# Kernel optimization log

Measured on AMD Instinct MI355X. Metric: run time of the kernel, lower is better.

Reference implementation:

```python
import jax, jax.numpy as jnp
from jax import lax
import numpy as np

NUM_HEAD = 4
D_MODEL = 160
HEAD_DIM = D_MODEL // NUM_HEAD  # 40
FEAT_DIM = 64
F_SIZE = (128, 128)
B = 4
LN_EPS = 1e-5
LEAKY_SLOPE = 0.01
DN = ('NCHW', 'OIHW', 'NCHW')


def setup_inputs() -> dict:
    key = jax.random.key(0)
    ks = jax.random.split(key, 10)
    pe_len = (F_SIZE[0] // 2) * (F_SIZE[1] // 2) + 1  # 4097
    s = 0.05
    return {
        'x': jax.random.normal(ks[0], (B, FEAT_DIM, F_SIZE[0], F_SIZE[1]), jnp.float32),
        'conv1_w': jax.random.normal(ks[1], (FEAT_DIM, FEAT_DIM, 2, 2), jnp.float32) * s,
        'conv1_b': jax.random.normal(ks[2], (FEAT_DIM,), jnp.float32) * s,
        'conv2_w': jax.random.normal(ks[3], (D_MODEL, FEAT_DIM, 1, 1), jnp.float32) * s,
        'conv2_b': jax.random.normal(ks[4], (D_MODEL,), jnp.float32) * s,
        'pe': jax.random.uniform(ks[5], (pe_len, 1), jnp.float32),
        'wq': jax.random.normal(ks[6], (D_MODEL, D_MODEL), jnp.float32) * s,
        'wk': jax.random.normal(ks[7], (D_MODEL, D_MODEL), jnp.float32) * s,
        'wv': jax.random.normal(ks[8], (D_MODEL, D_MODEL), jnp.float32) * s,
        'ln_w': jnp.ones((D_MODEL,), jnp.float32),
        'ln_b': jnp.zeros((D_MODEL,), jnp.float32),
    }


def reference(x, conv1_w, conv1_b, conv2_w, conv2_b, pe, wq, wk, wv, ln_w, ln_b):
    b = x.shape[0]
    # patch embed: stride-2 conv -> 1x1 conv -> LeakyReLU
    f = lax.conv_general_dilated(x, conv1_w, (2, 2), 'VALID', dimension_numbers=DN)
    f = f + conv1_b[None, :, None, None]
    f = lax.conv_general_dilated(f, conv2_w, (1, 1), 'VALID', dimension_numbers=DN)
    f = f + conv2_b[None, :, None, None]
    f = jnp.where(f >= 0, f, LEAKY_SLOPE * f)
    _, c, h, w = f.shape  # [b, 160, 64, 64]
    f = f.reshape(b, c, h * w).transpose(0, 2, 1)  # [b, s, d]
    # pad one extra token at end of sequence, add positional encoding [s+1, 1]
    f = jnp.pad(f, ((0, 0), (0, 1), (0, 0))) + pe  # [b, s+1, d]
    s1 = f.shape[1]
    # torch Linear (no bias): y = x @ W.T
    q = (f @ wq.T).reshape(b, s1, NUM_HEAD, HEAD_DIM).transpose(0, 2, 1, 3)
    k = (f @ wk.T).reshape(b, s1, NUM_HEAD, HEAD_DIM).transpose(0, 2, 1, 3)
    v = (f @ wv.T).reshape(b, s1, NUM_HEAD, HEAD_DIM).transpose(0, 2, 1, 3)
    score = jnp.einsum('bhqd,bhkd->bhqk', q, k) / jnp.sqrt(jnp.float32(HEAD_DIM))
    score = jax.nn.softmax(score, axis=-1)
    att = jnp.einsum('bhqk,bhkd->bhqd', score, v)  # [b, h, s+1, hd]
    cat = att.transpose(0, 2, 1, 3).reshape(b, s1, D_MODEL)
    feat = cat[:, :-1, :]  # drop padded token -> [b, s, d]
    # residual LayerNorm: LN(feat) + feat
    mu = jnp.mean(feat, axis=-1, keepdims=True)
    var = jnp.mean(jnp.square(feat - mu), axis=-1, keepdims=True)
    ln = (feat - mu) / jnp.sqrt(var + LN_EPS) * ln_w + ln_b
    feat = ln + feat
    feat = feat.transpose(0, 2, 1).reshape(b, D_MODEL, h, w)  # [b, 160, 64, 64]
    feat = jnp.repeat(jnp.repeat(feat, 2, axis=2), 2, axis=3)
    return feat
```

## Files before the change

### kernel.cpp

```cpp
#include <hip/hip_runtime.h>

typedef _Float16 f16;
typedef _Float16 half2v __attribute__((ext_vector_type(2)));
typedef _Float16 half4v __attribute__((ext_vector_type(4)));
typedef _Float16 half8 __attribute__((ext_vector_type(8)));
typedef float f32x4 __attribute__((ext_vector_type(4)));

#define MFMA16(a, b, c) __builtin_amdgcn_mfma_f32_16x16x32_f16((a), (b), (c), 0, 0, 0)

__device__ __forceinline__ unsigned pk2(float a, float b) {
  return __builtin_bit_cast(unsigned, __builtin_amdgcn_cvt_pkrtz(a, b));
}


__global__ __launch_bounds__(256) void k_convqkv(
    const float* __restrict__ x, const float* __restrict__ w1, const float* __restrict__ b1,
    const float* __restrict__ w2, const float* __restrict__ b2, const float* __restrict__ pe,
    const float* __restrict__ wq, const float* __restrict__ wk, const float* __restrict__ wv,
    f16* __restrict__ q_h, f16* __restrict__ k_h, f16* __restrict__ vt_h,
    float* __restrict__ kmaxp) {
  __shared__ __attribute__((aligned(16))) char smem[112192];
  f16* fT   = (f16*)smem;
  f16* xh   = (f16*)(smem + 21504);
  f16* wT   = (f16*)(smem + 21504);
  float* red = (float*)(smem + 48384);
  f16* w1h  = (f16*)(smem + 55360);
  f16* c1t  = (f16*)(smem + 55360);
  float* red160 = (float*)(smem + 64576);
  f16* w2h  = (f16*)(smem + 89152);

  int y = blockIdx.x, b = blockIdx.y;
  int t = threadIdx.x, lane = t & 63, wv4 = t >> 6, quad = lane >> 4, col = lane & 15;
  int s0 = y * 64;

  const float* xb = x + (b * 64) * 16384 + (2 * y) * 128;
#pragma unroll
  for (int it = 0; it < 32; ++it) {
    int flat = t + it * 256;
    int pos = flat & 63, r = (flat >> 6) & 1, ci = flat >> 7;
    float2 v = *(const float2*)(xb + ci * 16384 + r * 128 + 2 * pos);
    *(unsigned*)(xh + pos * 264 + ci * 4 + r * 2) = pk2(v.x, v.y);
  }
#pragma unroll
  for (int it = 0; it < 16; ++it) {
    int i4 = t + it * 256;
    int co = i4 >> 6, q4 = (i4 & 63) * 4;
    f32x4 v = *(const f32x4*)(w1 + co * 256 + q4);
    uint2 u = {pk2(v[0], v[1]), pk2(v[2], v[3])};
    *(uint2*)(w1h + co * 264 + q4) = u;
  }
#pragma unroll
  for (int it = 0; it < 10; ++it) {
    int i4 = t + it * 256;
    int c2 = i4 >> 4, q4 = (i4 & 15) * 4;
    f32x4 v = *(const f32x4*)(w2 + c2 * 160 / 160 * 0 + c2 * 64 + q4);
    uint2 u = {pk2(v[0], v[1]), pk2(v[2], v[3])};
    *(uint2*)(w2h + c2 * 72 + q4) = u;
  }
  __syncthreads();

  float b1v[4];
#pragma unroll
  for (int r = 0; r < 4; ++r) b1v[r] = b1[wv4 * 16 + quad * 4 + r];
  f32x4 acc1[4];
#pragma unroll
  for (int nt = 0; nt < 4; ++nt)
#pragma unroll
    for (int r = 0; r < 4; ++r) acc1[nt][r] = b1v[r];
#pragma unroll
  for (int kk = 0; kk < 8; ++kk) {
    half8 a = *(half8*)(w1h + (wv4 * 16 + col) * 264 + kk * 32 + quad * 8);
#pragma unroll
    for (int nt = 0; nt < 4; ++nt) {
      half8 bfr = *(half8*)(xh + (nt * 16 + col) * 264 + kk * 32 + quad * 8);
      acc1[nt] = MFMA16(a, bfr, acc1[nt]);
    }
  }
  __syncthreads();
#pragma unroll
  for (int nt = 0; nt < 4; ++nt) {
    uint2 u = {pk2(acc1[nt][0], acc1[nt][1]), pk2(acc1[nt][2], acc1[nt][3])};
    *(uint2*)(c1t + (nt * 16 + col) * 72 + wv4 * 16 + quad * 4) = u;
  }
  __syncthreads();

  f32x4 acc2[10];
#pragma unroll
  for (int mt = 0; mt < 10; ++mt)
#pragma unroll
    for (int r = 0; r < 4; ++r) acc2[mt][r] = b2[mt * 16 + quad * 4 + r];
  half8 bb0 = *(half8*)(c1t + (wv4 * 16 + col) * 72 + quad * 8);
  half8 bb1 = *(half8*)(c1t + (wv4 * 16 + col) * 72 + 32 + quad * 8);
#pragma unroll
  for (int mt = 0; mt < 10; ++mt) {
    half8 a0 = *(half8*)(w2h + (mt * 16 + col) * 72 + quad * 8);
    half8 a1 = *(half8*)(w2h + (mt * 16 + col) * 72 + 32 + quad * 8);
    acc2[mt] = MFMA16(a0, bb0, acc2[mt]);
    acc2[mt] = MFMA16(a1, bb1, acc2[mt]);
  }
  float pes = pe[s0 + wv4 * 16 + col];
#pragma unroll
  for (int mt = 0; mt < 10; ++mt) {
    float p[4];
#pragma unroll
    for (int r = 0; r < 4; ++r) {
      float v = acc2[mt][r];
      v = (v >= 0.f) ? v : 0.01f * v;
      p[r] = v + pes;
    }
    uint2 u = {pk2(p[0], p[1]), pk2(p[2], p[3])};
    *(uint2*)(fT + (wv4 * 16 + col) * 168 + mt * 16 + quad * 4) = u;
  }
  __syncthreads();

  half8 af[5];
  int rowA = wv4 * 16 + col;
#pragma unroll
  for (int kk = 0; kk < 5; ++kk)
    af[kk] = *(half8*)(fT + rowA * 168 + kk * 32 + quad * 8);

  float ks0[4], ks1[4];
#pragma unroll
  for (int r = 0; r < 4; ++r) { ks0[r] = 0.f; ks1[r] = 0.f; }

  for (int kind = 0; kind < 3; ++kind) {
    const float* wsp = (kind == 0) ? wq : (kind == 1 ? wk : wv);
    for (int hf = 0; hf < 2; ++hf) {
      __syncthreads();
      for (int c = t; c < 1600; c += 256) {
        int row = c / 20, seg = c - row * 20;
        const float* src = wsp + (hf * 80 + row) * 160 + seg * 8;
        f32x4 va = *(const f32x4*)src;
        f32x4 vb = *(const f32x4*)(src + 4);
        uint4 u = {pk2(va[0], va[1]), pk2(va[2], va[3]), pk2(vb[0], vb[1]), pk2(vb[2], vb[3])};
        *(uint4*)(wT + row * 168 + seg * 8) = u;
      }
      __syncthreads();
#pragma unroll
      for (int n0 = 0; n0 < 5; ++n0) {
        f32x4 acc; acc[0] = 0.f; acc[1] = 0.f; acc[2] = 0.f; acc[3] = 0.f;
        int rowB = n0 * 16 + col;
#pragma unroll
        for (int kk = 0; kk < 5; ++kk) {
          half8 bf = *(half8*)(wT + rowB * 168 + kk * 32 + quad * 8);
          acc = MFMA16(af[kk], bf, acc);
        }
        int o = (hf * 5 + n0) * 16 + col;
        int hh = o / 40, d = o - hh * 40;
        int bh = b * 4 + hh;
        if (kind == 1) {
          bool kidx = (n0 * 16 + col) >= 40;
#pragma unroll
          for (int r = 0; r < 4; ++r) {
            float z = acc[r] * acc[r];
            ks0[r] += kidx ? 0.f : z;
            ks1[r] += kidx ? z : 0.f;
          }
        }
#pragma unroll
        for (int r = 0; r < 4; ++r) {
          int s = s0 + wv4 * 16 + quad * 4 + r;
          f16 v = (f16)acc[r];
          if (kind == 0)      q_h[((size_t)bh * 4097 + s) * 40 + d] = v;
          else if (kind == 1) k_h[((size_t)bh * 4160 + s) * 40 + d] = v;
          else                vt_h[((size_t)bh * 40 + d) * 4160 + s] = v;
        }
      }
      if (kind == 1) {
        float m0 = 0.f, m1 = 0.f;
#pragma unroll
        for (int r = 0; r < 4; ++r) {
          float v0 = ks0[r], v1 = ks1[r];
          v0 += __shfl_xor(v0, 1); v0 += __shfl_xor(v0, 2);
          v0 += __shfl_xor(v0, 4); v0 += __shfl_xor(v0, 8);
          v1 += __shfl_xor(v1, 1); v1 += __shfl_xor(v1, 2);
          v1 += __shfl_xor(v1, 4); v1 += __shfl_xor(v1, 8);
          m0 = fmaxf(m0, v0); m1 = fmaxf(m1, v1);
          ks0[r] = 0.f; ks1[r] = 0.f;
        }
        m0 = fmaxf(m0, __shfl_xor(m0, 16)); m0 = fmaxf(m0, __shfl_xor(m0, 32));
        m1 = fmaxf(m1, __shfl_xor(m1, 16)); m1 = fmaxf(m1, __shfl_xor(m1, 32));
        if (lane == 0) { red[wv4 * 4 + hf * 2] = m0; red[wv4 * 4 + hf * 2 + 1] = m1; }
      }
    }
  }
  __syncthreads();
  if (t < 4) {
    float m = fmaxf(fmaxf(red[t], red[4 + t]), fmaxf(red[8 + t], red[12 + t]));
    kmaxp[(b * 4 + t) * 65 + y] = m;
  }

  if (y == 63) {
    float pe4 = pe[4096];
    if (t < 160) {
      int hh = t / 40, d = t - hh * 40, bh = b * 4 + hh;
#pragma unroll
      for (int kind = 0; kind < 3; ++kind) {
        const float* wsp = (kind == 0) ? wq : (kind == 1 ? wk : wv);
        const float* wr = wsp + t * 160;
        float rs = 0.f;
#pragma unroll
        for (int c4 = 0; c4 < 40; ++c4) {
          f32x4 v = *(const f32x4*)(wr + c4 * 4);
          rs += v[0] + v[1] + v[2] + v[3];
        }
        float val = pe4 * rs;
        if (kind == 0)      q_h[((size_t)bh * 4097 + 4096) * 40 + d] = (f16)val;
        else if (kind == 1) { k_h[((size_t)bh * 4160 + 4096) * 40 + d] = (f16)val;
                              red160[t] = val * val; }
        else                vt_h[((size_t)bh * 40 + d) * 4160 + 4096] = (f16)val;
      }
    }
    __syncthreads();
    if (t < 4) {
      float s = 0.f;
#pragma unroll
      for (int j = 0; j < 40; ++j) s += red160[t * 40 + j];
      kmaxp[(b * 4 + t) * 65 + 64] = s;
    }
  }
}

__global__ __launch_bounds__(256, 4) void k_attn(
    const f16* __restrict__ q_h, const f16* __restrict__ k_h,
    const f16* __restrict__ vt_h, const float* __restrict__ kmaxp,
    float* __restrict__ pacc) {
  __shared__ __attribute__((aligned(16))) f16 Ks[2][64 * 40];
  __shared__ __attribute__((aligned(16))) f16 Vs[2][40 * 72];
  __shared__ __attribute__((aligned(16))) f16 Ps[4 * 32 * 72];
  __shared__ __attribute__((aligned(16))) f16 Ones[8];
  __shared__ __attribute__((aligned(16))) f16 Zro[8];
  __shared__ __attribute__((aligned(16))) float red4[4];

  int qt = blockIdx.x, bh = blockIdx.y, ks = blockIdx.z;
  int qbase = qt * 128;
  int t = threadIdx.x, lane = t & 63, wv = t >> 6, quad = lane >> 4, col = lane & 15;
  const float c1l = 0.15811388300841898f * 1.4426950408889634f;
  int gbase = ks * 33;
  int nIter = 33 - ks;

  const f16* qb = q_h + ((size_t)bh * 4097 + qbase) * 40;
  for (int c = t; c < 640; c += 256)
    *(uint4*)(Ps + c * 8) = *(const uint4*)(qb + c * 8);
  if (t < 8) { Zro[t] = (f16)0; Ones[t] = (f16)1; }
  {
    float vm = (t < 65) ? kmaxp[bh * 65 + t] : 0.f;
#pragma unroll
    for (int d = 1; d < 64; d <<= 1) vm = fmaxf(vm, __shfl_xor(vm, d));
    if (lane == 0) red4[wv] = vm;
  }

  const f16* khb = k_h + ((size_t)bh * 4160 + gbase * 64) * 40;
  const f16* vtb = vt_h + (size_t)bh * 40 * 4160;
  int vrow = t >> 3, vseg = t & 7;
  uint4 rka = *(const uint4*)(khb + t * 8);
  uint4 rkb = {0, 0, 0, 0}, rvb = {0, 0, 0, 0};
  if (t < 64) rkb = *(const uint4*)(khb + (256 + t) * 8);
  uint4 rva = *(const uint4*)(vtb + vrow * 4160 + gbase * 64 + vseg * 8);
  if (t < 64) rvb = *(const uint4*)(vtb + (32 + vrow) * 4160 + gbase * 64 + vseg * 8);
  __syncthreads();

  float mk = fmaxf(fmaxf(red4[0], red4[1]), fmaxf(red4[2], red4[3]));

  half8 bq[2][2];
  float mfl[2];
#pragma unroll
  for (int nt = 0; nt < 2; ++nt) {
    int row = wv * 32 + nt * 16 + col;
    bq[nt][0] = *(half8*)(Ps + row * 40 + quad * 8);
    const f16* p1 = (quad == 0) ? (Ps + row * 40 + 32) : Zro;
    bq[nt][1] = *(half8*)p1;
    float s = 0.f;
#pragma unroll
    for (int j = 0; j < 8; ++j) {
      float a0 = (float)bq[nt][0][j], a1 = (float)bq[nt][1][j];
      s += a0 * a0 + a1 * a1;
    }
    s += __shfl_xor(s, 16);
    s += __shfl_xor(s, 32);
    mfl[nt] = sqrtf(s * mk) * c1l - 14.0f;
  }

  f32x4 o_[2][3];
#pragma unroll
  for (int a = 0; a < 2; ++a)
#pragma unroll
    for (int b2 = 0; b2 < 3; ++b2)
#pragma unroll
      for (int r = 0; r < 4; ++r) o_[a][b2][r] = 0.f;

  f16* Pw = Ps + wv * (32 * 72);

  for (int kt = 0; kt < nIter; ++kt) {
    int bsel = kt & 1;
    int g = gbase + kt;
    *(uint4*)(&Ks[bsel][t * 8]) = rka;
    if (t < 64) *(uint4*)(&Ks[bsel][(256 + t) * 8]) = rkb;
    *(uint4*)(&Vs[bsel][vrow * 72 + vseg * 8]) = rva;
    if (t < 64) *(uint4*)(&Vs[bsel][(32 + vrow) * 72 + vseg * 8]) = rvb;
    if (kt + 1 < nIter) {
      const f16* kn = khb + (size_t)(kt + 1) * 2560;
      int k0n = (g + 1) << 6;
      rka = *(const uint4*)(kn + t * 8);
      if (t < 64) rkb = *(const uint4*)(kn + (256 + t) * 8);
      rva = *(const uint4*)(vtb + vrow * 4160 + k0n + vseg * 8);
      if (t < 64) rvb = *(const uint4*)(vtb + (32 + vrow) * 4160 + k0n + vseg * 8);
    }
    __syncthreads();

    f32x4 acc[4][2];
#pragma unroll
    for (int mt = 0; mt < 4; ++mt) {
      int row = mt * 16 + col;
      half8 ak0 = *(half8*)(&Ks[bsel][row * 40 + quad * 8]);
      const f16* pa1 = (quad == 0) ? &Ks[bsel][row * 40 + 32] : Zro;
      half8 ak1 = *(half8*)pa1;
#pragma unroll
      for (int nt = 0; nt < 2; ++nt) {
        f32x4 a; a[0] = 0.f; a[1] = 0.f; a[2] = 0.f; a[3] = 0.f;
        a = MFMA16(ak0, bq[nt][0], a);
        a = MFMA16(ak1, bq[nt][1], a);
        acc[mt][nt] = a;
      }
    }
    bool lastt = (g == 64);
#pragma unroll
    for (int mt = 0; mt < 4; ++mt)
#pragma unroll
      for (int nt = 0; nt < 2; ++nt) {
        float p[4];
#pragma unroll
        for (int r = 0; r < 4; ++r) {
          p[r] = __builtin_amdgcn_exp2f(fmaf(acc[mt][nt][r], c1l, -mfl[nt]));
          if (lastt && (mt * 16 + quad * 4 + r) != 0) p[r] = 0.f;
        }
        half2v lo = __builtin_bit_cast(half2v, __builtin_amdgcn_cvt_pkrtz(p[0], p[1]));
        half2v hi = __builtin_bit_cast(half2v, __builtin_amdgcn_cvt_pkrtz(p[2], p[3]));
        half4v pk; pk.lo = lo; pk.hi = hi;
        *(half4v*)(Pw + (nt * 16 + col) * 72 + mt * 16 + quad * 4) = pk;
      }
#pragma unroll
    for (int kk2 = 0; kk2 < 2; ++kk2) {
      half8 ap0 = *(half8*)(Pw + col * 72 + kk2 * 32 + quad * 8);
      half8 ap1 = *(half8*)(Pw + (16 + col) * 72 + kk2 * 32 + quad * 8);
#pragma unroll
      for (int nv = 0; nv < 3; ++nv) {
        int d = nv * 16 + col;
        const f16* vp = (d < 40) ? &Vs[bsel][d * 72 + kk2 * 32 + quad * 8]
                                 : ((d == 40) ? Ones : Zro);
        half8 bv = *(half8*)vp;
        o_[0][nv] = MFMA16(ap0, bv, o_[0][nv]);
        o_[1][nv] = MFMA16(ap1, bv, o_[1][nv]);
      }
    }
  }

  float* pb = pacc + (size_t)(ks * 16 + bh) * 4096 * 48;
#pragma unroll
  for (int mtq = 0; mtq < 2; ++mtq)
#pragma unroll
    for (int nv = 0; nv < 3; ++nv)
#pragma unroll
      for (int r = 0; r < 4; ++r) {
        int q = qbase + wv * 32 + mtq * 16 + quad * 4 + r;
        pb[(size_t)q * 48 + nv * 16 + col] = o_[mtq][nv][r];
      }
}

__global__ __launch_bounds__(256) void k_ln_out(
    const float* __restrict__ pacc, const float* __restrict__ lnw,
    const float* __restrict__ lnb, float* __restrict__ out) {
  __shared__ float g[32 * 164];
  __shared__ float linv[32 * 4];
  int y = blockIdx.x, b = blockIdx.y, z = blockIdx.z, t = threadIdx.x;
  const size_t P1 = (size_t)16 * 4096 * 48;
  int w0 = z * 32;
  if (t < 128) {
    int row = t >> 2, h = t & 3;
    size_t i0 = ((size_t)(b * 4 + h) * 4096 + y * 64 + w0 + row) * 48 + 40;
    linv[row * 4 + h] = 1.f / (pacc[i0] + pacc[P1 + i0]);
  }
  __syncthreads();
#pragma unroll
  for (int it = 0; it < 5; ++it) {
    int flat = t + it * 256;
    int row = flat / 40, dq = flat - row * 40;
    int h = dq / 10, d = (dq - h * 10) * 4;
    size_t idx = ((size_t)(b * 4 + h) * 4096 + y * 64 + w0 + row) * 48 + d;
    f32x4 v0 = *(const f32x4*)(pacc + idx);
    f32x4 v1 = *(const f32x4*)(pacc + P1 + idx);
    float li = linv[row * 4 + h];
    f32x4 gv;
#pragma unroll
    for (int j = 0; j < 4; ++j) gv[j] = (v0[j] + v1[j]) * li;
    *(f32x4*)(g + row * 164 + h * 40 + d) = gv;
  }
  __syncthreads();
  int row = t >> 3, part = t & 7;
  float* gr = g + row * 164 + part * 20;
  float s1 = 0.f, s2 = 0.f;
#pragma unroll
  for (int j4 = 0; j4 < 5; ++j4) {
    f32x4 v = *(f32x4*)(gr + j4 * 4);
#pragma unroll
    for (int j = 0; j < 4; ++j) { s1 += v[j]; s2 += v[j] * v[j]; }
  }
  s1 += __shfl_xor(s1, 1); s1 += __shfl_xor(s1, 2); s1 += __shfl_xor(s1, 4);
  s2 += __shfl_xor(s2, 1); s2 += __shfl_xor(s2, 2); s2 += __shfl_xor(s2, 4);
  float mu = s1 * (1.f / 160.f);
  float var = s2 * (1.f / 160.f) - mu * mu;
  float inv = rsqrtf(var + 1e-5f);
  const float* lw = lnw + part * 20;
  const float* lb = lnb + part * 20;
#pragma unroll
  for (int j = 0; j < 20; ++j) {
    float v = gr[j];
    gr[j] = (v - mu) * inv * lw[j] + lb[j] + v;
  }
  __syncthreads();
  int Yo = t >> 7, xp = t & 63, cpar = (t >> 6) & 1;
  int rl = xp >> 1;
  float* ob = out + (2 * y + Yo) * 128 + z * 64 + xp;
  for (int c = cpar; c < 160; c += 2)
    ob[(size_t)(b * 160 + c) * 16384] = g[rl * 164 + c];
}

extern "C" void kernel_launch(void* const* d_in, const int* in_sizes, int n_in,
                              void* d_out, int out_size, void* d_ws, size_t ws_size,
                              hipStream_t stream) {
  const float* x   = (const float*)d_in[0];
  const float* w1  = (const float*)d_in[1];
  const float* b1  = (const float*)d_in[2];
  const float* w2  = (const float*)d_in[3];
  const float* b2  = (const float*)d_in[4];
  const float* pe  = (const float*)d_in[5];
  const float* wq  = (const float*)d_in[6];
  const float* wk  = (const float*)d_in[7];
  const float* wvp = (const float*)d_in[8];
  const float* lnw = (const float*)d_in[9];
  const float* lnb = (const float*)d_in[10];
  float* out = (float*)d_out;

  char* p = (char*)d_ws;
  f16* q_h   = (f16*)p;   p += (size_t)16 * 4097 * 40 * 2;
  f16* k_h   = (f16*)p;   p += (size_t)16 * 4160 * 40 * 2;
  f16* vt_h  = (f16*)p;   p += (size_t)16 * 40 * 4160 * 2;
  float* pacc = (float*)p; p += (size_t)2 * 16 * 4096 * 48 * 4;
  float* kmaxp = (float*)p; p += 16 * 65 * 4;

  k_convqkv<<<dim3(64, 4), 256, 0, stream>>>(x, w1, b1, w2, b2, pe, wq, wk, wvp,
                                             q_h, k_h, vt_h, kmaxp);
  k_attn<<<dim3(32, 16, 2), 256, 0, stream>>>(q_h, k_h, vt_h, kmaxp, pacc);
  k_ln_out<<<dim3(64, 4, 2), 256, 0, stream>>>(pacc, lnw, lnb, out);
}
```

Measured before the change: 220.6 us.

## Keep softmax probabilities in registers via permlane swaps instead of LDS round-trip

The attention kernel no longer writes the exp'd score tile P to shared memory and reads it back as the MFMA A-operand. It uses v_permlane32_swap/v_permlane16_swap to rearrange the score accumulator layout directly into the operand layout, and interleaves QK and PV per 32-key half. Q fragments are now loaded straight from global memory into registers rather than staged through LDS. This removes the LDS traffic and the Ps buffer, which frees shared memory for occupancy. It relies on gfx950 permlane swap instructions and an inline-asm s_nop hazard guard, so the lane mapping must be exactly right.

```diff
diff --git a/kernel.cpp b/kernel.cpp
--- a/kernel.cpp
+++ b/kernel.cpp
@@ -5,11 +5,19 @@
 typedef _Float16 half4v __attribute__((ext_vector_type(4)));
 typedef _Float16 half8 __attribute__((ext_vector_type(8)));
 typedef float f32x4 __attribute__((ext_vector_type(4)));
+typedef unsigned u32x4 __attribute__((ext_vector_type(4)));
 
 #define MFMA16(a, b, c) __builtin_amdgcn_mfma_f32_16x16x32_f16((a), (b), (c), 0, 0, 0)
 
 __device__ __forceinline__ unsigned pk2(float a, float b) {
   return __builtin_bit_cast(unsigned, __builtin_amdgcn_cvt_pkrtz(a, b));
+}
+
+__device__ __forceinline__ void plswap_pair(unsigned& a, unsigned& b) {
+  asm("s_nop 1\n\t"
+      "v_permlane32_swap_b32 %0, %1\n\t"
+      "v_permlane16_swap_b32 %0, %1"
+      : "+v"(a), "+v"(b));
 }
 
 
@@ -227,7 +235,6 @@
     float* __restrict__ pacc) {
   __shared__ __attribute__((aligned(16))) f16 Ks[2][64 * 40];
   __shared__ __attribute__((aligned(16))) f16 Vs[2][40 * 72];
-  __shared__ __attribute__((aligned(16))) f16 Ps[4 * 32 * 72];
   __shared__ __attribute__((aligned(16))) f16 Ones[8];
   __shared__ __attribute__((aligned(16))) f16 Zro[8];
   __shared__ __attribute__((aligned(16))) float red4[4];
@@ -239,9 +246,6 @@
   int gbase = ks * 33;
   int nIter = 33 - ks;
 
-  const f16* qb = q_h + ((size_t)bh * 4097 + qbase) * 40;
-  for (int c = t; c < 640; c += 256)
-    *(uint4*)(Ps + c * 8) = *(const uint4*)(qb + c * 8);
   if (t < 8) { Zro[t] = (f16)0; Ones[t] = (f16)1; }
   {
     float vm = (t < 65) ? kmaxp[bh * 65 + t] : 0.f;
@@ -258,18 +262,25 @@
   if (t < 64) rkb = *(const uint4*)(khb + (256 + t) * 8);
   uint4 rva = *(const uint4*)(vtb + vrow * 4160 + gbase * 64 + vseg * 8);
   if (t < 64) rvb = *(const uint4*)(vtb + (32 + vrow) * 4160 + gbase * 64 + vseg * 8);
+
+  half8 zero8;
+#pragma unroll
+  for (int j = 0; j < 8; ++j) zero8[j] = (f16)0;
+
+  half8 bq[2][2];
+#pragma unroll
+  for (int nt = 0; nt < 2; ++nt) {
+    const f16* qr = q_h + ((size_t)bh * 4097 + qbase + wv * 32 + nt * 16 + col) * 40;
+    bq[nt][0] = *(const half8*)(qr + quad * 8);
+    bq[nt][1] = (quad == 0) ? *(const half8*)(qr + 32) : zero8;
+  }
   __syncthreads();
 
   float mk = fmaxf(fmaxf(red4[0], red4[1]), fmaxf(red4[2], red4[3]));
 
-  half8 bq[2][2];
   float mfl[2];
 #pragma unroll
   for (int nt = 0; nt < 2; ++nt) {
-    int row = wv * 32 + nt * 16 + col;
-    bq[nt][0] = *(half8*)(Ps + row * 40 + quad * 8);
-    const f16* p1 = (quad == 0) ? (Ps + row * 40 + 32) : Zro;
-    bq[nt][1] = *(half8*)p1;
     float s = 0.f;
 #pragma unroll
     for (int j = 0; j < 8; ++j) {
@@ -288,8 +299,6 @@
     for (int b2 = 0; b2 < 3; ++b2)
 #pragma unroll
       for (int r = 0; r < 4; ++r) o_[a][b2][r] = 0.f;
-
-  f16* Pw = Ps + wv * (32 * 72);
 
   for (int kt = 0; kt < nIter; ++kt) {
     int bsel = kt & 1;
@@ -308,49 +317,54 @@
     }
     __syncthreads();
 
-    f32x4 acc[4][2];
-#pragma unroll
-    for (int mt = 0; mt < 4; ++mt) {
-      int row = mt * 16 + col;
-      half8 ak0 = *(half8*)(&Ks[bsel][row * 40 + quad * 8]);
-      const f16* pa1 = (quad == 0) ? &Ks[bsel][row * 40 + 32] : Zro;
-      half8 ak1 = *(half8*)pa1;
+    bool lastt = (g == 64);
+#pragma unroll
+    for (int kk2 = 0; kk2 < 2; ++kk2) {
+      f32x4 acc[2][2];
+#pragma unroll
+      for (int hf = 0; hf < 2; ++hf) {
+        int mt = kk2 * 2 + hf;
+        int row = mt * 16 + col;
+        half8 ak0 = *(half8*)(&Ks[bsel][row * 40 + quad * 8]);
+        const f16* pa1 = (quad == 0) ? &Ks[bsel][row * 40 + 32] : Zro;
+        half8 ak1 = *(half8*)pa1;
+#pragma unroll
+        for (int nt = 0; nt < 2; ++nt) {
+          f32x4 a; a[0] = 0.f; a[1] = 0.f; a[2] = 0.f; a[3] = 0.f;
+          a = MFMA16(ak0, bq[nt][0], a);
+          a = MFMA16(ak1, bq[nt][1], a);
+          acc[hf][nt] = a;
+        }
+      }
+      half8 pa[2];
 #pragma unroll
       for (int nt = 0; nt < 2; ++nt) {
-        f32x4 a; a[0] = 0.f; a[1] = 0.f; a[2] = 0.f; a[3] = 0.f;
-        a = MFMA16(ak0, bq[nt][0], a);
-        a = MFMA16(ak1, bq[nt][1], a);
-        acc[mt][nt] = a;
-      }
-    }
-    bool lastt = (g == 64);
-#pragma unroll
-    for (int mt = 0; mt < 4; ++mt)
-#pragma unroll
-      for (int nt = 0; nt < 2; ++nt) {
-        float p[4];
-#pragma unroll
-        for (int r = 0; r < 4; ++r) {
-          p[r] = __builtin_amdgcn_exp2f(fmaf(acc[mt][nt][r], c1l, -mfl[nt]));
-          if (lastt && (mt * 16 + quad * 4 + r) != 0) p[r] = 0.f;
-        }
-        half2v lo = __builtin_bit_cast(half2v, __builtin_amdgcn_cvt_pkrtz(p[0], p[1]));
-        half2v hi = __builtin_bit_cast(half2v, __builtin_amdgcn_cvt_pkrtz(p[2], p[3]));
-        half4v pk; pk.lo = lo; pk.hi = hi;
-        *(half4v*)(Pw + (nt * 16 + col) * 72 + mt * 16 + quad * 4) = pk;
-      }
-#pragma unroll
-    for (int kk2 = 0; kk2 < 2; ++kk2) {
-      half8 ap0 = *(half8*)(Pw + col * 72 + kk2 * 32 + quad * 8);
-      half8 ap1 = *(half8*)(Pw + (16 + col) * 72 + kk2 * 32 + quad * 8);
+        unsigned sr[4];
+#pragma unroll
+        for (int hf = 0; hf < 2; ++hf) {
+          int mt = kk2 * 2 + hf;
+          float p[4];
+#pragma unroll
+          for (int r = 0; r < 4; ++r) {
+            p[r] = __builtin_amdgcn_exp2f(fmaf(acc[hf][nt][r], c1l, -mfl[nt]));
+            if (lastt && (mt * 16 + quad * 4 + r) != 0) p[r] = 0.f;
+          }
+          sr[hf * 2]     = pk2(p[0], p[1]);
+          sr[hf * 2 + 1] = pk2(p[2], p[3]);
+        }
+        plswap_pair(sr[0], sr[2]);
+        plswap_pair(sr[1], sr[3]);
+        u32x4 uu; uu[0] = sr[0]; uu[1] = sr[1]; uu[2] = sr[2]; uu[3] = sr[3];
+        pa[nt] = __builtin_bit_cast(half8, uu);
+      }
 #pragma unroll
       for (int nv = 0; nv < 3; ++nv) {
         int d = nv * 16 + col;
         const f16* vp = (d < 40) ? &Vs[bsel][d * 72 + kk2 * 32 + quad * 8]
                                  : ((d == 40) ? Ones : Zro);
         half8 bv = *(half8*)vp;
-        o_[0][nv] = MFMA16(ap0, bv, o_[0][nv]);
-        o_[1][nv] = MFMA16(ap1, bv, o_[1][nv]);
+        o_[0][nv] = MFMA16(pa[0], bv, o_[0][nv]);
+        o_[1][nv] = MFMA16(pa[1], bv, o_[1][nv]);
       }
     }
   }
```

New measurement: 214.3 us. -2.9%, faster.
